# Kernel optimization log

Measured on AMD Instinct MI355X. Metric: run time of the kernel, lower is better.

## Reference

```python
import jax, jax.numpy as jnp
import numpy as np

N_NODES = 20000
N_EDGES = 160000
D_IN = 512
D_OUT = 64


def _propagate(x, src, dst, num_nodes):
    # SLPropagate with add_self_loops=False, normalize=False:
    # out[dst] += x[src]  (plain sum aggregation over incoming edges)
    return jax.ops.segment_sum(x[src], dst, num_segments=num_nodes)


def setup_inputs() -> dict:
    key = jax.random.key(0)
    k1, k2, k3, k4 = jax.random.split(key, 4)
    x = jax.random.normal(k1, (N_NODES, D_IN), dtype=jnp.float32)
    edge_index = jax.random.randint(k2, (2, N_EDGES), 0, N_NODES, dtype=jnp.int64)
    # torch.nn.Linear default init scale ~ 1/sqrt(fan_in)
    s = 1.0 / np.sqrt(D_IN)
    W1 = jax.random.uniform(k3, (D_IN, D_IN), dtype=jnp.float32, minval=-s, maxval=s)
    W2 = jax.random.uniform(k4, (D_OUT, D_IN), dtype=jnp.float32, minval=-s, maxval=s)
    return {"x": x, "edge_index": edge_index, "W1": W1, "W2": W2}


def reference(x, edge_index, W1, W2):
    num_nodes = x.shape[0]
    src, dst = edge_index[0], edge_index[1]
    h = _propagate(x, src, dst, num_nodes)          # [N, D_IN]
    h = jax.nn.relu(jnp.einsum('nd,ed->ne', h, W1))  # lin1 (no bias) + relu
    h = _propagate(h, src, dst, num_nodes)          # [N, D_IN]
    h = jnp.einsum('nd,od->no', h, W2)              # lin2 (no bias) -> [N, D_OUT]
    return jax.nn.log_softmax(h, axis=1)
```

## Files before the change

### kernel.cpp

```cpp
#include <hip/hip_runtime.h>

#define D 512
#define DOUT 64

typedef __bf16 bf16x8 __attribute__((ext_vector_type(8)));
typedef float floatx4 __attribute__((ext_vector_type(4)));

__device__ __forceinline__ void async_cp16(const void* g, void* lds) {
    __builtin_amdgcn_global_load_lds(
        (__attribute__((address_space(1))) void*)(void*)g,
        (__attribute__((address_space(3))) void*)lds, 16, 0, 0);
}

__global__ __launch_bounds__(256) void misc_kernel(
        const int* __restrict__ dst, int* __restrict__ deg, int nE, int degBlocks,
        const float* __restrict__ x, __bf16* __restrict__ xb, int xN8,
        const float* __restrict__ W1, __bf16* __restrict__ w1b, int w1N8,
        const float* __restrict__ W2, __bf16* __restrict__ w2b, int w2N8) {
    int b = blockIdx.x;
    if (b < degBlocks) {
        int e = b * 256 + threadIdx.x;
        if (e < nE) atomicAdd(&deg[dst[e]], 1);
        return;
    }
    b -= degBlocks;
    int xBlocks = (xN8 + 255) >> 8;
    int w1Blocks = (w1N8 + 255) >> 8;
    const float* in; __bf16* outp; int n8;
    if (b < xBlocks) { in = x; outp = xb; n8 = xN8; }
    else if (b < xBlocks + w1Blocks) { b -= xBlocks; in = W1; outp = w1b; n8 = w1N8; }
    else { b -= xBlocks + w1Blocks; in = W2; outp = w2b; n8 = w2N8; }
    int i = b * 256 + threadIdx.x;
    if (i < n8) {
        const float4* p = (const float4*)in + (size_t)i * 2;
        float4 v0 = p[0], v1 = p[1];
        bf16x8 o;
        o[0] = (__bf16)v0.x; o[1] = (__bf16)v0.y; o[2] = (__bf16)v0.z; o[3] = (__bf16)v0.w;
        o[4] = (__bf16)v1.x; o[5] = (__bf16)v1.y; o[6] = (__bf16)v1.z; o[7] = (__bf16)v1.w;
        *((bf16x8*)outp + i) = o;
    }
}

__global__ __launch_bounds__(1024) void exscan_kernel(const int* __restrict__ deg,
                                                      int* __restrict__ rp,
                                                      int* __restrict__ cursor, int n) {
    __shared__ int wtot[16];
    __shared__ int carry;
    int tid = threadIdx.x, lane = tid & 63, wid = tid >> 6;
    if (tid == 0) carry = 0;
    __syncthreads();
    for (int base = 0; base < n; base += 4096) {
        int i4 = base + tid * 4;
        int4 v = make_int4(0, 0, 0, 0);
        if (i4 + 3 < n) v = *(const int4*)(deg + i4);
        else {
            if (i4 + 0 < n) v.x = deg[i4 + 0];
            if (i4 + 1 < n) v.y = deg[i4 + 1];
            if (i4 + 2 < n) v.z = deg[i4 + 2];
            if (i4 + 3 < n) v.w = deg[i4 + 3];
        }
        int tsum = v.x + v.y + v.z + v.w;
        int s = tsum;
        #pragma unroll
        for (int off = 1; off < 64; off <<= 1) {
            int t = __shfl_up(s, off, 64);
            if (lane >= off) s += t;
        }
        if (lane == 63) wtot[wid] = s;
        __syncthreads();
        if (wid == 0 && lane < 16) {
            int wv = wtot[lane];
            int ws_ = wv;
            #pragma unroll
            for (int off = 1; off < 16; off <<= 1) {
                int t = __shfl_up(ws_, off, 64);
                if (lane >= off) ws_ += t;
            }
            wtot[lane] = ws_ - wv;
        }
        __syncthreads();
        int excl = carry + wtot[wid] + (s - tsum);
        int4 o;
        o.x = excl; o.y = o.x + v.x; o.z = o.y + v.y; o.w = o.z + v.z;
        if (i4 + 3 < n) {
            *(int4*)(rp + i4) = o;
            *(int4*)(cursor + i4) = o;
        } else {
            if (i4 + 0 < n) { rp[i4 + 0] = o.x; cursor[i4 + 0] = o.x; }
            if (i4 + 1 < n) { rp[i4 + 1] = o.y; cursor[i4 + 1] = o.y; }
            if (i4 + 2 < n) { rp[i4 + 2] = o.z; cursor[i4 + 2] = o.z; }
            if (i4 + 3 < n) { rp[i4 + 3] = o.w; cursor[i4 + 3] = o.w; }
        }
        __syncthreads();
        if (tid == 1023) carry = o.w + v.w;
        __syncthreads();
    }
    if (tid == 0) rp[n] = carry;
}

__global__ void fill_kernel(const int* __restrict__ src, const int* __restrict__ dst,
                            int* __restrict__ cursor, int* __restrict__ col, int nE) {
    int e = blockIdx.x * blockDim.x + threadIdx.x;
    if (e < nE) {
        int d = dst[e];
        int p = atomicAdd(&cursor[d], 1);
        col[p] = src[e];
    }
}

template<bool RELU>
__global__ __launch_bounds__(256) void propagate_bf16(const __bf16* __restrict__ xin,
        const int* __restrict__ rp, const int* __restrict__ col,
        __bf16* __restrict__ out, int nN) {
    int n = blockIdx.x * 4 + (threadIdx.x >> 6);
    if (n >= nN) return;
    int lane = threadIdx.x & 63;
    int s0 = rp[n], s1 = rp[n + 1];
    float acc0[8] = {}, acc1[8] = {};
    int e = s0;
    for (; e + 4 <= s1; e += 4) {
        int sa = col[e], sb = col[e + 1], sc = col[e + 2], sd = col[e + 3];
        bf16x8 va = *(const bf16x8*)(xin + (size_t)sa * D + lane * 8);
        bf16x8 vb = *(const bf16x8*)(xin + (size_t)sb * D + lane * 8);
        bf16x8 vc = *(const bf16x8*)(xin + (size_t)sc * D + lane * 8);
        bf16x8 vd = *(const bf16x8*)(xin + (size_t)sd * D + lane * 8);
        #pragma unroll
        for (int i = 0; i < 8; ++i) {
            acc0[i] += (float)va[i] + (float)vc[i];
            acc1[i] += (float)vb[i] + (float)vd[i];
        }
    }
    for (; e < s1; ++e) {
        int sa = col[e];
        bf16x8 va = *(const bf16x8*)(xin + (size_t)sa * D + lane * 8);
        #pragma unroll
        for (int i = 0; i < 8; ++i) acc0[i] += (float)va[i];
    }
    bf16x8 o;
    #pragma unroll
    for (int i = 0; i < 8; ++i) {
        float v = acc0[i] + acc1[i];
        if (RELU) v = fmaxf(v, 0.f);
        o[i] = (__bf16)v;
    }
    *(bf16x8*)(out + (size_t)n * D + lane * 8) = o;
}

template<int BM, int BN, int WR, int WC, bool RELU>
__global__ __launch_bounds__(256) void gemm_mfma_nt(
        const __bf16* __restrict__ A, const __bf16* __restrict__ B,
        __bf16* __restrict__ Cout, int M, int N, int K) {
    constexpr int BK = 32;
    constexpr int WM = BM / WR, WN = BN / WC;
    constexpr int MI = WM / 16, NI = WN / 16;
    constexpr int CPA = BM / 64, CPB = BN / 64;

    __shared__ __bf16 As[4 * BM * 8];
    __shared__ __bf16 Bs[4 * BN * 8];

    const int tid = threadIdx.x;
    const int w = tid >> 6, lane = tid & 63;
    const int wrow = w / WC, wcol = w % WC;
    const int m0 = blockIdx.y * BM, n0 = blockIdx.x * BN;
    const int quad = lane >> 4, l15 = lane & 15;

    floatx4 acc[MI][NI] = {};

    for (int k0 = 0; k0 < K; k0 += BK) {
        #pragma unroll
        for (int c = 0; c < CPA; ++c) {
            int ca = w * CPA + c;
            int kq = ca / CPA;
            int row = m0 + (ca % CPA) * 64 + lane;
            if (row > M - 1) row = M - 1;
            async_cp16(A + (size_t)row * K + k0 + kq * 8, &As[(size_t)ca * 512]);
        }
        #pragma unroll
        for (int c = 0; c < CPB; ++c) {
            int cb = w * CPB + c;
            int kq = cb / CPB;
            int nn = n0 + (cb % CPB) * 64 + lane;
            async_cp16(B + (size_t)nn * K + k0 + kq * 8, &Bs[(size_t)cb * 512]);
        }
        __syncthreads();

        bf16x8 af[MI], bfr[NI];
        #pragma unroll
        for (int mi = 0; mi < MI; ++mi)
            af[mi] = *(const bf16x8*)&As[(size_t)(quad * BM + wrow * WM + mi * 16 + l15) * 8];
        #pragma unroll
        for (int nj = 0; nj < NI; ++nj)
            bfr[nj] = *(const bf16x8*)&Bs[(size_t)(quad * BN + wcol * WN + nj * 16 + l15) * 8];
        #pragma unroll
        for (int mi = 0; mi < MI; ++mi)
            #pragma unroll
            for (int nj = 0; nj < NI; ++nj)
                acc[mi][nj] = __builtin_amdgcn_mfma_f32_16x16x32_bf16(
                    af[mi], bfr[nj], acc[mi][nj], 0, 0, 0);
        __syncthreads();
    }

    #pragma unroll
    for (int mi = 0; mi < MI; ++mi) {
        #pragma unroll
        for (int r = 0; r < 4; ++r) {
            int m = m0 + wrow * WM + mi * 16 + quad * 4 + r;
            if (m < M) {
                #pragma unroll
                for (int nj = 0; nj < NI; ++nj) {
                    int n = n0 + wcol * WN + nj * 16 + l15;
                    float v = acc[mi][nj][r];
                    if (RELU) v = fmaxf(v, 0.f);
                    Cout[(size_t)m * N + n] = (__bf16)v;
                }
            }
        }
    }
}

__global__ __launch_bounds__(256) void prop2_lsm(const __bf16* __restrict__ u,
        const int* __restrict__ rp, const int* __restrict__ col,
        float* __restrict__ out, int nN) {
    int n = blockIdx.x * 4 + (threadIdx.x >> 6);
    if (n >= nN) return;
    int lane = threadIdx.x & 63;
    int s0 = rp[n], s1 = rp[n + 1];
    float a0 = 0.f, a1 = 0.f, a2 = 0.f, a3 = 0.f;
    int e = s0;
    for (; e + 4 <= s1; e += 4) {
        int sa = col[e], sb = col[e + 1], sc = col[e + 2], sd = col[e + 3];
        a0 += (float)u[(size_t)sa * DOUT + lane];
        a1 += (float)u[(size_t)sb * DOUT + lane];
        a2 += (float)u[(size_t)sc * DOUT + lane];
        a3 += (float)u[(size_t)sd * DOUT + lane];
    }
    for (; e < s1; ++e) a0 += (float)u[(size_t)col[e] * DOUT + lane];
    float v = (a0 + a2) + (a1 + a3);
    float mx = v;
    #pragma unroll
    for (int off = 32; off >= 1; off >>= 1) mx = fmaxf(mx, __shfl_xor(mx, off, 64));
    float s = expf(v - mx);
    #pragma unroll
    for (int off = 32; off >= 1; off >>= 1) s += __shfl_xor(s, off, 64);
    out[(size_t)n * DOUT + lane] = v - mx - logf(s);
}


extern "C" void kernel_launch(void* const* d_in, const int* in_sizes, int n_in,
                              void* d_out, int out_size, void* d_ws, size_t ws_size,
                              hipStream_t stream) {
    const float* x  = (const float*)d_in[0];
    const int*   ei = (const int*)d_in[1];
    const float* W1 = (const float*)d_in[2];
    const float* W2 = (const float*)d_in[3];
    float* out = (float*)d_out;

    const int N = in_sizes[0] / D;
    const int E = in_sizes[1] / 2;
    const int* src = ei;
    const int* dst = ei + E;

    size_t off = 0;
    auto alloc = [&](size_t bytes) -> void* {
        void* p = (char*)d_ws + off;
        off = (off + bytes + 255) & ~(size_t)255;
        return p;
    };
    int*    deg     = (int*)alloc(sizeof(int) * (size_t)N);
    int*    row_ptr = (int*)alloc(sizeof(int) * (size_t)(N + 1));
    int*    cursor  = (int*)alloc(sizeof(int) * (size_t)N);
    int*    col     = (int*)alloc(sizeof(int) * (size_t)E);
    __bf16* w1b     = (__bf16*)alloc(sizeof(__bf16) * (size_t)D * D);
    __bf16* w2b     = (__bf16*)alloc(sizeof(__bf16) * (size_t)DOUT * D);
    __bf16* xb      = (__bf16*)alloc(sizeof(__bf16) * (size_t)N * D);
    __bf16* t       = (__bf16*)alloc(sizeof(__bf16) * (size_t)N * D);
    __bf16* h2      = (__bf16*)alloc(sizeof(__bf16) * (size_t)N * D);
    __bf16* u       = (__bf16*)alloc(sizeof(__bf16) * (size_t)N * DOUT);

    const int degBlocks = (E + 255) / 256;
    const int xN8 = N * D / 8, w1N8 = D * D / 8, w2N8 = DOUT * D / 8;
    const int cvtBlocks = (xN8 + 255) / 256 + (w1N8 + 255) / 256 + (w2N8 + 255) / 256;

    hipMemsetAsync(deg, 0, sizeof(int) * (size_t)N, stream);
    misc_kernel<<<degBlocks + cvtBlocks, 256, 0, stream>>>(
        dst, deg, E, degBlocks, x, xb, xN8, W1, w1b, w1N8, W2, w2b, w2N8);
    exscan_kernel<<<1, 1024, 0, stream>>>(deg, row_ptr, cursor, N);
    fill_kernel<<<(E + 255) / 256, 256, 0, stream>>>(src, dst, cursor, col, E);

    dim3 g1(D / 128, (N + 127) / 128);
    gemm_mfma_nt<128, 128, 2, 2, false><<<g1, 256, 0, stream>>>(xb, w1b, t, N, D, D);
    propagate_bf16<true><<<(N + 3) / 4, 256, 0, stream>>>(t, row_ptr, col, h2, N);
    dim3 g2(1, (N + 63) / 64);
    gemm_mfma_nt<64, 64, 2, 2, false><<<g2, 256, 0, stream>>>(h2, w2b, u, N, DOUT, D);
    prop2_lsm<<<(N + 3) / 4, 256, 0, stream>>>(u, row_ptr, col, out, N);
}
```

Measured before the change: 188.5 us.

## Merge CSR build into cooperative kernel and fuse first propagate with lin2 GEMM

```diff
diff --git a/kernel.cpp b/kernel.cpp
--- a/kernel.cpp
+++ b/kernel.cpp
@@ -1,7 +1,11 @@
 #include <hip/hip_runtime.h>
+#include <hip/hip_cooperative_groups.h>
+
+namespace cg = cooperative_groups;
 
 #define D 512
 #define DOUT 64
+#define PREP_BLOCKS 256
 
 typedef __bf16 bf16x8 __attribute__((ext_vector_type(8)));
 typedef float floatx4 __attribute__((ext_vector_type(4)));
@@ -12,52 +16,48 @@
         (__attribute__((address_space(3))) void*)lds, 16, 0, 0);
 }
 
-__global__ __launch_bounds__(256) void misc_kernel(
-        const int* __restrict__ dst, int* __restrict__ deg, int nE, int degBlocks,
+__device__ __forceinline__ void cvt8(const float* __restrict__ in,
+                                     __bf16* __restrict__ out, int i) {
+    const float4* p = (const float4*)in + (size_t)i * 2;
+    float4 v0 = p[0], v1 = p[1];
+    bf16x8 o;
+    o[0] = (__bf16)v0.x; o[1] = (__bf16)v0.y; o[2] = (__bf16)v0.z; o[3] = (__bf16)v0.w;
+    o[4] = (__bf16)v1.x; o[5] = (__bf16)v1.y; o[6] = (__bf16)v1.z; o[7] = (__bf16)v1.w;
+    *((bf16x8*)out + i) = o;
+}
+
+__global__ __launch_bounds__(256) void coop_prep(
+        const int* __restrict__ src, const int* __restrict__ dst,
+        int* __restrict__ deg, int* __restrict__ rp, int* __restrict__ cursor,
+        int* __restrict__ col, int* __restrict__ bsum,
         const float* __restrict__ x, __bf16* __restrict__ xb, int xN8,
         const float* __restrict__ W1, __bf16* __restrict__ w1b, int w1N8,
-        const float* __restrict__ W2, __bf16* __restrict__ w2b, int w2N8) {
-    int b = blockIdx.x;
-    if (b < degBlocks) {
-        int e = b * 256 + threadIdx.x;
-        if (e < nE) atomicAdd(&deg[dst[e]], 1);
-        return;
-    }
-    b -= degBlocks;
-    int xBlocks = (xN8 + 255) >> 8;
-    int w1Blocks = (w1N8 + 255) >> 8;
-    const float* in; __bf16* outp; int n8;
-    if (b < xBlocks) { in = x; outp = xb; n8 = xN8; }
-    else if (b < xBlocks + w1Blocks) { b -= xBlocks; in = W1; outp = w1b; n8 = w1N8; }
-    else { b -= xBlocks + w1Blocks; in = W2; outp = w2b; n8 = w2N8; }
-    int i = b * 256 + threadIdx.x;
-    if (i < n8) {
-        const float4* p = (const float4*)in + (size_t)i * 2;
-        float4 v0 = p[0], v1 = p[1];
-        bf16x8 o;
-        o[0] = (__bf16)v0.x; o[1] = (__bf16)v0.y; o[2] = (__bf16)v0.z; o[3] = (__bf16)v0.w;
-        o[4] = (__bf16)v1.x; o[5] = (__bf16)v1.y; o[6] = (__bf16)v1.z; o[7] = (__bf16)v1.w;
-        *((bf16x8*)outp + i) = o;
-    }
-}
-
-__global__ __launch_bounds__(1024) void exscan_kernel(const int* __restrict__ deg,
-                                                      int* __restrict__ rp,
-                                                      int* __restrict__ cursor, int n) {
-    __shared__ int wtot[16];
-    __shared__ int carry;
-    int tid = threadIdx.x, lane = tid & 63, wid = tid >> 6;
-    if (tid == 0) carry = 0;
-    __syncthreads();
-    for (int base = 0; base < n; base += 4096) {
-        int i4 = base + tid * 4;
+        const float* __restrict__ W2, __bf16* __restrict__ w2b, int w2N8,
+        int nN, int nE) {
+    cg::grid_group grid = cg::this_grid();
+    const int tid = threadIdx.x, b = blockIdx.x;
+    const int lane = tid & 63, wid = tid >> 6;
+    const int gidx = b * 256 + tid, gsz = gridDim.x * 256;
+
+    for (int i = gidx; i < nN; i += gsz) deg[i] = 0;
+    for (int i = gidx; i < xN8; i += gsz) cvt8(x, xb, i);
+    for (int i = gidx; i < w1N8; i += gsz) cvt8(W1, w1b, i);
+    for (int i = gidx; i < w2N8; i += gsz) cvt8(W2, w2b, i);
+    grid.sync();
+
+    for (int e = gidx; e < nE; e += gsz) atomicAdd(&deg[dst[e]], 1);
+    grid.sync();
+
+    const int nChunks = (nN + 1023) >> 10;
+    __shared__ int wtot[4];
+    const int i4 = b * 1024 + tid * 4;
+    if (b < nChunks) {
         int4 v = make_int4(0, 0, 0, 0);
-        if (i4 + 3 < n) v = *(const int4*)(deg + i4);
+        if (i4 + 3 < nN) v = *(const int4*)(deg + i4);
         else {
-            if (i4 + 0 < n) v.x = deg[i4 + 0];
-            if (i4 + 1 < n) v.y = deg[i4 + 1];
-            if (i4 + 2 < n) v.z = deg[i4 + 2];
-            if (i4 + 3 < n) v.w = deg[i4 + 3];
+            if (i4 + 0 < nN) v.x = deg[i4 + 0];
+            if (i4 + 1 < nN) v.y = deg[i4 + 1];
+            if (i4 + 2 < nN) v.z = deg[i4 + 2];
         }
         int tsum = v.x + v.y + v.z + v.w;
         int s = tsum;
@@ -68,82 +68,51 @@
         }
         if (lane == 63) wtot[wid] = s;
         __syncthreads();
-        if (wid == 0 && lane < 16) {
-            int wv = wtot[lane];
-            int ws_ = wv;
-            #pragma unroll
-            for (int off = 1; off < 16; off <<= 1) {
-                int t = __shfl_up(ws_, off, 64);
-                if (lane >= off) ws_ += t;
-            }
-            wtot[lane] = ws_ - wv;
-        }
-        __syncthreads();
-        int excl = carry + wtot[wid] + (s - tsum);
+        int woff = 0, btot = 0;
+        #pragma unroll
+        for (int i = 0; i < 4; ++i) {
+            if (i < wid) woff += wtot[i];
+            btot += wtot[i];
+        }
+        if (tid == 0) bsum[b] = btot;
+        int excl = woff + (s - tsum);
         int4 o;
         o.x = excl; o.y = o.x + v.x; o.z = o.y + v.y; o.w = o.z + v.z;
-        if (i4 + 3 < n) {
-            *(int4*)(rp + i4) = o;
-            *(int4*)(cursor + i4) = o;
-        } else {
-            if (i4 + 0 < n) { rp[i4 + 0] = o.x; cursor[i4 + 0] = o.x; }
-            if (i4 + 1 < n) { rp[i4 + 1] = o.y; cursor[i4 + 1] = o.y; }
-            if (i4 + 2 < n) { rp[i4 + 2] = o.z; cursor[i4 + 2] = o.z; }
-            if (i4 + 3 < n) { rp[i4 + 3] = o.w; cursor[i4 + 3] = o.w; }
-        }
-        __syncthreads();
-        if (tid == 1023) carry = o.w + v.w;
-        __syncthreads();
-    }
-    if (tid == 0) rp[n] = carry;
-}
-
-__global__ void fill_kernel(const int* __restrict__ src, const int* __restrict__ dst,
-                            int* __restrict__ cursor, int* __restrict__ col, int nE) {
-    int e = blockIdx.x * blockDim.x + threadIdx.x;
-    if (e < nE) {
+        if (i4 + 3 < nN) *(int4*)(rp + i4) = o;
+        else {
+            if (i4 + 0 < nN) rp[i4 + 0] = o.x;
+            if (i4 + 1 < nN) rp[i4 + 1] = o.y;
+            if (i4 + 2 < nN) rp[i4 + 2] = o.z;
+        }
+    }
+    grid.sync();
+
+    if (b == 0 && tid == 0) {
+        int run = 0;
+        for (int i = 0; i < nChunks; ++i) { int t = bsum[i]; bsum[i] = run; run += t; }
+        rp[nN] = run;
+    }
+    grid.sync();
+
+    if (b < nChunks) {
+        int add = bsum[b];
+        #pragma unroll
+        for (int j = 0; j < 4; ++j) {
+            int i = i4 + j;
+            if (i < nN) {
+                int val = rp[i] + add;
+                rp[i] = val;
+                cursor[i] = val;
+            }
+        }
+    }
+    grid.sync();
+
+    for (int e = gidx; e < nE; e += gsz) {
         int d = dst[e];
         int p = atomicAdd(&cursor[d], 1);
         col[p] = src[e];
     }
-}
-
-template<bool RELU>
-__global__ __launch_bounds__(256) void propagate_bf16(const __bf16* __restrict__ xin,
-        const int* __restrict__ rp, const int* __restrict__ col,
-        __bf16* __restrict__ out, int nN) {
-    int n = blockIdx.x * 4 + (threadIdx.x >> 6);
-    if (n >= nN) return;
-    int lane = threadIdx.x & 63;
-    int s0 = rp[n], s1 = rp[n + 1];
-    float acc0[8] = {}, acc1[8] = {};
-    int e = s0;
-    for (; e + 4 <= s1; e += 4) {
-        int sa = col[e], sb = col[e + 1], sc = col[e + 2], sd = col[e + 3];
-        bf16x8 va = *(const bf16x8*)(xin + (size_t)sa * D + lane * 8);
-        bf16x8 vb = *(const bf16x8*)(xin + (size_t)sb * D + lane * 8);
-        bf16x8 vc = *(const bf16x8*)(xin + (size_t)sc * D + lane * 8);
-        bf16x8 vd = *(const bf16x8*)(xin + (size_t)sd * D + lane * 8);
-        #pragma unroll
-        for (int i = 0; i < 8; ++i) {
-            acc0[i] += (float)va[i] + (float)vc[i];
-            acc1[i] += (float)vb[i] + (float)vd[i];
-        }
-    }
-    for (; e < s1; ++e) {
-        int sa = col[e];
-        bf16x8 va = *(const bf16x8*)(xin + (size_t)sa * D + lane * 8);
-        #pragma unroll
-        for (int i = 0; i < 8; ++i) acc0[i] += (float)va[i];
-    }
-    bf16x8 o;
-    #pragma unroll
-    for (int i = 0; i < 8; ++i) {
-        float v = acc0[i] + acc1[i];
-        if (RELU) v = fmaxf(v, 0.f);
-        o[i] = (__bf16)v;
-    }
-    *(bf16x8*)(out + (size_t)n * D + lane * 8) = o;
 }
 
 template<int BM, int BN, int WR, int WC, bool RELU>
@@ -214,6 +183,78 @@
                     Cout[(size_t)m * N + n] = (__bf16)v;
                 }
             }
+        }
+    }
+}
+
+__global__ __launch_bounds__(256) void prop1_gemm2(
+        const __bf16* __restrict__ t, const int* __restrict__ rp,
+        const int* __restrict__ col, const __bf16* __restrict__ B,
+        __bf16* __restrict__ u, int nN) {
+    __shared__ __bf16 As[32 * 512];
+    __shared__ __bf16 Bs[4 * 64 * 8];
+
+    const int tid = threadIdx.x;
+    const int w = tid >> 6, lane = tid & 63;
+    const int quad = lane >> 4, l15 = lane & 15;
+    const int wrow = w >> 1, wcol = w & 1;
+    const int m0 = blockIdx.x * 32;
+
+    for (int r = w; r < 32; r += 4) {
+        int n = m0 + r;
+        float acc0[8] = {}, acc1[8] = {};
+        if (n < nN) {
+            int s0 = rp[n], s1 = rp[n + 1];
+            int e = s0;
+            for (; e + 4 <= s1; e += 4) {
+                int sa = col[e], sb = col[e + 1], sc = col[e + 2], sd = col[e + 3];
+                bf16x8 va = *(const bf16x8*)(t + (size_t)sa * D + lane * 8);
+                bf16x8 vb = *(const bf16x8*)(t + (size_t)sb * D + lane * 8);
+                bf16x8 vc = *(const bf16x8*)(t + (size_t)sc * D + lane * 8);
+                bf16x8 vd = *(const bf16x8*)(t + (size_t)sd * D + lane * 8);
+                #pragma unroll
+                for (int i = 0; i < 8; ++i) {
+                    acc0[i] += (float)va[i] + (float)vc[i];
+                    acc1[i] += (float)vb[i] + (float)vd[i];
+                }
+            }
+            for (; e < s1; ++e) {
+                int sa = col[e];
+                bf16x8 va = *(const bf16x8*)(t + (size_t)sa * D + lane * 8);
+                #pragma unroll
+                for (int i = 0; i < 8; ++i) acc0[i] += (float)va[i];
+            }
+        }
+        bf16x8 o;
+        #pragma unroll
+        for (int i = 0; i < 8; ++i) o[i] = (__bf16)fmaxf(acc0[i] + acc1[i], 0.f);
+        int P = r * 64 + ((lane + r) & 63);
+        *(bf16x8*)&As[(size_t)P * 8] = o;
+    }
+    __syncthreads();
+
+    floatx4 acc[2] = {};
+    for (int k0 = 0; k0 < D; k0 += 32) {
+        async_cp16(B + (size_t)lane * D + k0 + w * 8, &Bs[(size_t)w * 512]);
+        __syncthreads();
+        int g = (k0 >> 3) + quad;
+        int row = wrow * 16 + l15;
+        bf16x8 af = *(const bf16x8*)&As[(size_t)(row * 64 + ((g + row) & 63)) * 8];
+        #pragma unroll
+        for (int nj = 0; nj < 2; ++nj) {
+            bf16x8 bfr = *(const bf16x8*)&Bs[(size_t)(quad * 64 + wcol * 32 + nj * 16 + l15) * 8];
+            acc[nj] = __builtin_amdgcn_mfma_f32_16x16x32_bf16(af, bfr, acc[nj], 0, 0, 0);
+        }
+        __syncthreads();
+    }
+
+    #pragma unroll
+    for (int r = 0; r < 4; ++r) {
+        int m = m0 + wrow * 16 + quad * 4 + r;
+        if (m < nN) {
+            #pragma unroll
+            for (int nj = 0; nj < 2; ++nj)
+                u[(size_t)m * DOUT + wcol * 32 + nj * 16 + l15] = (__bf16)acc[nj][r];
         }
     }
 }
@@ -255,8 +296,8 @@
     const float* W2 = (const float*)d_in[3];
     float* out = (float*)d_out;
 
-    const int N = in_sizes[0] / D;
-    const int E = in_sizes[1] / 2;
+    int N = in_sizes[0] / D;
+    int E = in_sizes[1] / 2;
     const int* src = ei;
     const int* dst = ei + E;
 
@@ -270,27 +311,26 @@
     int*    row_ptr = (int*)alloc(sizeof(int) * (size_t)(N + 1));
     int*    cursor  = (int*)alloc(sizeof(int) * (size_t)N);
     int*    col     = (int*)alloc(sizeof(int) * (size_t)E);
+    int*    bsum    = (int*)alloc(sizeof(int) * 256);
     __bf16* w1b     = (__bf16*)alloc(sizeof(__bf16) * (size_t)D * D);
     __bf16* w2b     = (__bf16*)alloc(sizeof(__bf16) * (size_t)DOUT * D);
     __bf16* xb      = (__bf16*)alloc(sizeof(__bf16) * (size_t)N * D);
     __bf16* t       = (__bf16*)alloc(sizeof(__bf16) * (size_t)N * D);
-    __bf16* h2      = (__bf16*)alloc(sizeof(__bf16) * (size_t)N * D);
     __bf16* u       = (__bf16*)alloc(sizeof(__bf16) * (size_t)N * DOUT);
 
-    const int degBlocks = (E + 255) / 256;
-    const int xN8 = N * D / 8, w1N8 = D * D / 8, w2N8 = DOUT * D / 8;
-    const int cvtBlocks = (xN8 + 255) / 256 + (w1N8 + 255) / 256 + (w2N8 + 255) / 256;
-
-    hipMemsetAsync(deg, 0, sizeof(int) * (size_t)N, stream);
-    misc_kernel<<<degBlocks + cvtBlocks, 256, 0, stream>>>(
-        dst, deg, E, degBlocks, x, xb, xN8, W1, w1b, w1N8, W2, w2b, w2N8);
-    exscan_kernel<<<1, 1024, 0, stream>>>(deg, row_ptr, cursor, N);
-    fill_kernel<<<(E + 255) / 256, 256, 0, stream>>>(src, dst, cursor, col, E);
+    int xN8 = N * D / 8, w1N8 = D * D / 8, w2N8 = DOUT * D / 8;
+
+    void* args[] = { (void*)&src, (void*)&dst, (void*)&deg, (void*)&row_ptr,
+                     (void*)&cursor, (void*)&col, (void*)&bsum,
+                     (void*)&x, (void*)&xb, (void*)&xN8,
+                     (void*)&W1, (void*)&w1b, (void*)&w1N8,
+                     (void*)&W2, (void*)&w2b, (void*)&w2N8,
+                     (void*)&N, (void*)&E };
+    hipLaunchCooperativeKernel((void*)coop_prep, dim3(PREP_BLOCKS), dim3(256),
+                               args, 0, stream);
 
     dim3 g1(D / 128, (N + 127) / 128);
     gemm_mfma_nt<128, 128, 2, 2, false><<<g1, 256, 0, stream>>>(xb, w1b, t, N, D, D);
-    propagate_bf16<true><<<(N + 3) / 4, 256, 0, stream>>>(t, row_ptr, col, h2, N);
-    dim3 g2(1, (N + 63) / 64);
-    gemm_mfma_nt<64, 64, 2, 2, false><<<g2, 256, 0, stream>>>(h2, w2b, u, N, DOUT, D);
+    prop1_gemm2<<<(N + 31) / 32, 256, 0, stream>>>(t, row_ptr, col, w2b, u, N);
     prop2_lsm<<<(N + 3) / 4, 256, 0, stream>>>(u, row_ptr, col, out, N);
 }
```

After: 343.4 us. 1.82x slower.

## Fuse first propagation with ReLU and second GEMM into one kernel

Applied to the files above, without the earlier changes.

```diff
diff --git a/kernel.cpp b/kernel.cpp
--- a/kernel.cpp
+++ b/kernel.cpp
@@ -108,44 +108,6 @@
     }
 }
 
-template<bool RELU>
-__global__ __launch_bounds__(256) void propagate_bf16(const __bf16* __restrict__ xin,
-        const int* __restrict__ rp, const int* __restrict__ col,
-        __bf16* __restrict__ out, int nN) {
-    int n = blockIdx.x * 4 + (threadIdx.x >> 6);
-    if (n >= nN) return;
-    int lane = threadIdx.x & 63;
-    int s0 = rp[n], s1 = rp[n + 1];
-    float acc0[8] = {}, acc1[8] = {};
-    int e = s0;
-    for (; e + 4 <= s1; e += 4) {
-        int sa = col[e], sb = col[e + 1], sc = col[e + 2], sd = col[e + 3];
-        bf16x8 va = *(const bf16x8*)(xin + (size_t)sa * D + lane * 8);
-        bf16x8 vb = *(const bf16x8*)(xin + (size_t)sb * D + lane * 8);
-        bf16x8 vc = *(const bf16x8*)(xin + (size_t)sc * D + lane * 8);
-        bf16x8 vd = *(const bf16x8*)(xin + (size_t)sd * D + lane * 8);
-        #pragma unroll
-        for (int i = 0; i < 8; ++i) {
-            acc0[i] += (float)va[i] + (float)vc[i];
-            acc1[i] += (float)vb[i] + (float)vd[i];
-        }
-    }
-    for (; e < s1; ++e) {
-        int sa = col[e];
-        bf16x8 va = *(const bf16x8*)(xin + (size_t)sa * D + lane * 8);
-        #pragma unroll
-        for (int i = 0; i < 8; ++i) acc0[i] += (float)va[i];
-    }
-    bf16x8 o;
-    #pragma unroll
-    for (int i = 0; i < 8; ++i) {
-        float v = acc0[i] + acc1[i];
-        if (RELU) v = fmaxf(v, 0.f);
-        o[i] = (__bf16)v;
-    }
-    *(bf16x8*)(out + (size_t)n * D + lane * 8) = o;
-}
-
 template<int BM, int BN, int WR, int WC, bool RELU>
 __global__ __launch_bounds__(256) void gemm_mfma_nt(
         const __bf16* __restrict__ A, const __bf16* __restrict__ B,
@@ -214,6 +176,78 @@
                     Cout[(size_t)m * N + n] = (__bf16)v;
                 }
             }
+        }
+    }
+}
+
+__global__ __launch_bounds__(256) void prop1_gemm2(
+        const __bf16* __restrict__ t, const int* __restrict__ rp,
+        const int* __restrict__ col, const __bf16* __restrict__ B,
+        __bf16* __restrict__ u, int nN) {
+    __shared__ __bf16 As[32 * 512];
+    __shared__ __bf16 Bs[4 * 64 * 8];
+
+    const int tid = threadIdx.x;
+    const int w = tid >> 6, lane = tid & 63;
+    const int quad = lane >> 4, l15 = lane & 15;
+    const int wrow = w >> 1, wcol = w & 1;
+    const int m0 = blockIdx.x * 32;
+
+    for (int r = w; r < 32; r += 4) {
+        int n = m0 + r;
+        float acc0[8] = {}, acc1[8] = {};
+        if (n < nN) {
+            int s0 = rp[n], s1 = rp[n + 1];
+            int e = s0;
+            for (; e + 4 <= s1; e += 4) {
+                int sa = col[e], sb = col[e + 1], sc = col[e + 2], sd = col[e + 3];
+                bf16x8 va = *(const bf16x8*)(t + (size_t)sa * D + lane * 8);
+                bf16x8 vb = *(const bf16x8*)(t + (size_t)sb * D + lane * 8);
+                bf16x8 vc = *(const bf16x8*)(t + (size_t)sc * D + lane * 8);
+                bf16x8 vd = *(const bf16x8*)(t + (size_t)sd * D + lane * 8);
+                #pragma unroll
+                for (int i = 0; i < 8; ++i) {
+                    acc0[i] += (float)va[i] + (float)vc[i];
+                    acc1[i] += (float)vb[i] + (float)vd[i];
+                }
+            }
+            for (; e < s1; ++e) {
+                int sa = col[e];
+                bf16x8 va = *(const bf16x8*)(t + (size_t)sa * D + lane * 8);
+                #pragma unroll
+                for (int i = 0; i < 8; ++i) acc0[i] += (float)va[i];
+            }
+        }
+        bf16x8 o;
+        #pragma unroll
+        for (int i = 0; i < 8; ++i) o[i] = (__bf16)fmaxf(acc0[i] + acc1[i], 0.f);
+        int P = r * 64 + ((lane + r) & 63);
+        *(bf16x8*)&As[(size_t)P * 8] = o;
+    }
+    __syncthreads();
+
+    floatx4 acc[2] = {};
+    for (int k0 = 0; k0 < D; k0 += 32) {
+        async_cp16(B + (size_t)lane * D + k0 + w * 8, &Bs[(size_t)w * 512]);
+        __syncthreads();
+        int g = (k0 >> 3) + quad;
+        int row = wrow * 16 + l15;
+        bf16x8 af = *(const bf16x8*)&As[(size_t)(row * 64 + ((g + row) & 63)) * 8];
+        #pragma unroll
+        for (int nj = 0; nj < 2; ++nj) {
+            bf16x8 bfr = *(const bf16x8*)&Bs[(size_t)(quad * 64 + wcol * 32 + nj * 16 + l15) * 8];
+            acc[nj] = __builtin_amdgcn_mfma_f32_16x16x32_bf16(af, bfr, acc[nj], 0, 0, 0);
+        }
+        __syncthreads();
+    }
+
+    #pragma unroll
+    for (int r = 0; r < 4; ++r) {
+        int m = m0 + wrow * 16 + quad * 4 + r;
+        if (m < nN) {
+            #pragma unroll
+            for (int nj = 0; nj < 2; ++nj)
+                u[(size_t)m * DOUT + wcol * 32 + nj * 16 + l15] = (__bf16)acc[nj][r];
         }
     }
 }
@@ -274,7 +308,6 @@
     __bf16* w2b     = (__bf16*)alloc(sizeof(__bf16) * (size_t)DOUT * D);
     __bf16* xb      = (__bf16*)alloc(sizeof(__bf16) * (size_t)N * D);
     __bf16* t       = (__bf16*)alloc(sizeof(__bf16) * (size_t)N * D);
-    __bf16* h2      = (__bf16*)alloc(sizeof(__bf16) * (size_t)N * D);
     __bf16* u       = (__bf16*)alloc(sizeof(__bf16) * (size_t)N * DOUT);
 
     const int degBlocks = (E + 255) / 256;
@@ -289,8 +322,6 @@
 
     dim3 g1(D / 128, (N + 127) / 128);
     gemm_mfma_nt<128, 128, 2, 2, false><<<g1, 256, 0, stream>>>(xb, w1b, t, N, D, D);
-    propagate_bf16<true><<<(N + 3) / 4, 256, 0, stream>>>(t, row_ptr, col, h2, N);
-    dim3 g2(1, (N + 63) / 64);
-    gemm_mfma_nt<64, 64, 2, 2, false><<<g2, 256, 0, stream>>>(h2, w2b, u, N, DOUT, D);
+    prop1_gemm2<<<(N + 31) / 32, 256, 0, stream>>>(t, row_ptr, col, w2b, u, N);
     prop2_lsm<<<(N + 3) / 4, 256, 0, stream>>>(u, row_ptr, col, out, N);
 }
```

After: 186.0 us. No clear change (-1.3%).
